# Kernel optimization log

Hardware: AMD Instinct MI355X
Metric: run time of the kernel (lower is better)

## Reference

```python
import jax, jax.numpy as jnp
import numpy as np

Z_DIM = 32
POLY_ORDER = 3
INCLUDE_BIAS = True

# Static index arrays replicating the nested-loop term ordering of the torch code.
_I2, _J2 = np.triu_indices(Z_DIM)  # pairs (i, j) with i <= j, row-major in i -> matches loop order
_TRIPLES = np.array([(i, j, k) for i in range(Z_DIM) for j in range(i, Z_DIM) for k in range(j, Z_DIM)], dtype=np.int32)
_TI, _TJ, _TK = _TRIPLES[:, 0], _TRIPLES[:, 1], _TRIPLES[:, 2]


def build_library(z):
    # z: [B, d] -> Theta: [B, n_terms], same column order as build_library_torch
    B = z.shape[0]
    terms = []
    if INCLUDE_BIAS:
        terms.append(jnp.ones((B, 1), dtype=z.dtype))
    terms.append(z)
    if POLY_ORDER >= 2:
        terms.append(z[:, _I2] * z[:, _J2])  # [B, C(d+1,2)] quadratic terms
    if POLY_ORDER >= 3:
        terms.append(z[:, _TI] * z[:, _TJ] * z[:, _TK])  # [B, C(d+2,3)] cubic terms
    return jnp.concatenate(terms, axis=1)


def setup_inputs() -> dict:
    key = jax.random.key(0)
    k1, k2 = jax.random.split(key)
    B = 65536
    n_terms = 6545  # 1 + 32 + 528 + 5984 for d=32, order=3, bias
    z = jax.random.normal(k1, (B, Z_DIM), dtype=jnp.float32)
    Xi = jax.random.normal(k2, (n_terms, Z_DIM), dtype=jnp.float32)
    Xi_mask = jnp.ones((n_terms, Z_DIM), dtype=jnp.float32)
    z_mean = jnp.zeros((1, Z_DIM), dtype=jnp.float32)
    z_std = jnp.ones((1, Z_DIM), dtype=jnp.float32)
    return {"z": z, "Xi": Xi, "Xi_mask": Xi_mask, "z_mean": z_mean, "z_std": z_std}


def reference(z, Xi, Xi_mask, z_mean, z_std):
    # NOTE: the original module computes z_norm = (z - z_mean) / z_std but
    # never uses it; Theta is built from the raw z. Reproduce exactly.
    Theta = build_library(z)            # [B, n_terms]
    Xi_eff = Xi * Xi_mask               # [n_terms, z_dim]
    dz_dt = Theta @ Xi_eff              # [B, z_dim]
    return dz_dt
```

## Files before the change

### kernel.cpp

```cpp
#include <hip/hip_runtime.h>


#define Z 32
#define ROWS 65536
#define NBLK (ROWS / 64)

#define NCHUNK 552
#define NGRAN (NCHUNK * 2)
#define NGP 1120
#define KSPAN 138

typedef short short8 __attribute__((ext_vector_type(8)));
typedef float f32x16 __attribute__((ext_vector_type(16)));
typedef float float2v __attribute__((ext_vector_type(2)));

struct Sched {
    unsigned mg[NGP];
    short rt[NGRAN * 8];
    int nq[4];
};

constexpr Sched make_sched() {
    Sched s{};
    short gi[NGP] = {}, gj[NGP] = {};
    char gt[NGP] = {}, gq[NGP] = {};
    int tidx[32][32] = {}, pidx[32] = {};
    {
        int n = 0;
        for (int a = 0; a < 32; ++a)
            for (int b = a; b < 32; ++b) { tidx[a][b] = n; n += 32 - b; }
        for (int i = 0; i < 32; ++i) pidx[i] = i * 32 - i * (i - 1) / 2;
    }
    int g = 0;
    for (int q = 0; q < 4; ++q) {
        int g0 = g;
        for (int b = 0; b < 32; ++b)
            if ((b >> 3) <= q)
                for (int a = 0; a <= b; ++a) { gi[g]=(short)a; gj[g]=(short)b; gt[g]=0; gq[g]=(char)q; ++g; }
        for (int b = 0; b < 32; ++b)
            if ((b >> 3) >= q) { gi[g]=(short)b; gj[g]=32; gt[g]=1; gq[g]=(char)q; ++g; }
        gi[g]=32; gj[g]=32; gt[g]=2; gq[g]=(char)q; ++g;
        while ((g - g0) & 7) { gi[g]=32; gj[g]=32; gt[g]=3; gq[g]=(char)q; ++g; }
        s.nq[q] = (g - g0) / 2;
    }
    for (int gg = 0; gg < NGRAN; ++gg) {
        s.mg[gg] = ((unsigned)gi[gg] * 256u) | (((unsigned)gj[gg] * 256u) << 16);
        int i = gi[gg], j = gj[gg], ty = gt[gg], q = gq[gg];
        for (int jj = 0; jj < 8; ++jj) {
            int k = 8 * q + jj, row = -1;
            if (ty == 0)      { if (k >= j) row = 561 + tidx[i][j] + (k - j); }
            else if (ty == 1) { if (k <= i) row = 33 + pidx[k] + (i - k); }
            else if (ty == 2) { row = 1 + k; }
            s.rt[gg * 8 + jj] = (short)row;
        }
    }
    return s;
}
constexpr Sched S = make_sched();
static_assert(S.nq[0] == 36 && S.nq[1] == 84 && S.nq[2] == 160 && S.nq[3] == 272, "chunk counts");

__device__ __forceinline__ unsigned pack_bf16(float s0, float s1) {
    return __builtin_amdgcn_perm(__builtin_bit_cast(unsigned, s1),
                                 __builtin_bit_cast(unsigned, s0), 0x07060302u);
}

__global__ void sindy_prep(const float* __restrict__ Xi,
                           const float* __restrict__ Xi_mask,
                           uint2* __restrict__ Bp2, size_t ws_size) {
    __shared__ unsigned short sh[8][32];
    const int tid = threadIdx.x;
    const int jj = tid >> 5, n = tid & 31;
#pragma unroll
    for (int pass = 0; pass < 4; ++pass) {
        int g = blockIdx.x * 4 + pass;
        int row = S.rt[g * 8 + jj];
        float f = 0.0f;
        if (row >= 0) f = Xi[row * Z + n] * Xi_mask[row * Z + n];
        unsigned u = __builtin_bit_cast(unsigned, f);
        sh[jj][n] = (unsigned short)((u + 0x7FFFu + ((u >> 16) & 1u)) >> 16);
        __syncthreads();
        if (tid < 64) {
            int n2 = tid & 31, rep = tid >> 5;
            unsigned v0 = sh[4*rep+0][n2], v1 = sh[4*rep+1][n2];
            unsigned v2 = sh[4*rep+2][n2], v3 = sh[4*rep+3][n2];
            int c = g >> 1, h = g & 1;
            size_t idx = ((size_t)c * 64 + h * 32 + n2) * 2 + rep;
            if ((idx + 1) * 8 <= ws_size)
                Bp2[idx] = uint2{v0 | (v1 << 16), v2 | (v3 << 16)};
        }
        __syncthreads();
    }
}

__global__ __launch_bounds__(256, 4) void sindy_mfma(const float* __restrict__ z,
                                                     const float* __restrict__ Xi,
                                                     const float* __restrict__ Xi_mask,
                                                     const uint4* __restrict__ Bp,
                                                     float* __restrict__ out) {
    const int lane = threadIdx.x & 63;
    const int kh = threadIdx.x >> 6;
    const int m = lane & 31;
    const int half = lane >> 5;
    const long R = (long)blockIdx.x * 64;

    __shared__ float zs[33][2][32];
    __shared__ float cs[3][2][32][32];
    __shared__ unsigned mg_sh[NGP];

    for (int t = threadIdx.x; t < NGP; t += 256) mg_sh[t] = S.mg[t];
    for (int idx = threadIdx.x; idx < 512; idx += 256) {
        int row = idx >> 3, q4 = idx & 7;
        float4 v = ((const float4*)(z + (R + row) * Z))[q4];
        int t = row >> 5, mm = row & 31;
        zs[4*q4+0][t][mm] = v.x; zs[4*q4+1][t][mm] = v.y;
        zs[4*q4+2][t][mm] = v.z; zs[4*q4+3][t][mm] = v.w;
    }
    if (threadIdx.x < 64) zs[32][threadIdx.x >> 5][threadIdx.x & 31] = 1.0f;
    __syncthreads();

    const int c0 = kh * KSPAN;
    const char* zmb = (const char*)&zs[0][0][0] + 4 * m;
    const unsigned* mgh = mg_sh + half;

    const uint4* p = Bp + lane + (size_t)c0 * 64;
    uint4 curA = p[0], curB = p[64];
    uint4 shA  = p[128], shB = p[192];

    unsigned u0 = mgh[2*c0], u1 = mgh[2*c0+2];
    float pA0, pA1, pB0, pB1;
    {
        float i0 = *(const float*)(zmb + (u0 & 0xFFFFu)), i1 = *(const float*)(zmb + (u0 & 0xFFFFu) + 128);
        float j0 = *(const float*)(zmb + (u0 >> 16)),     j1 = *(const float*)(zmb + (u0 >> 16) + 128);
        pA0 = i0 * j0; pA1 = i1 * j1;
        float e0 = *(const float*)(zmb + (u1 & 0xFFFFu)), e1 = *(const float*)(zmb + (u1 & 0xFFFFu) + 128);
        float f0 = *(const float*)(zmb + (u1 >> 16)),     f1 = *(const float*)(zmb + (u1 >> 16) + 128);
        pB0 = e0 * f0; pB1 = e1 * f1;
    }
    unsigned w0s = mgh[2*c0+4], w1s = mgh[2*c0+6];

    f32x16 acc0 = {}, acc1 = {};

    auto seg = [&](int Q, int cbeg, int cfin, bool lastp) {
        const char* zq = zmb + Q * 2048;
        float2v zA0, zA1, zA2, zA3, zB0, zB1, zB2, zB3;
        zA0.x = *(const float*)(zq +    0); zB0.x = *(const float*)(zq +  128);
        zA0.y = *(const float*)(zq +  256); zB0.y = *(const float*)(zq +  384);
        zA1.x = *(const float*)(zq +  512); zB1.x = *(const float*)(zq +  640);
        zA1.y = *(const float*)(zq +  768); zB1.y = *(const float*)(zq +  896);
        zA2.x = *(const float*)(zq + 1024); zB2.x = *(const float*)(zq + 1152);
        zA2.y = *(const float*)(zq + 1280); zB2.y = *(const float*)(zq + 1408);
        zA3.x = *(const float*)(zq + 1536); zB3.x = *(const float*)(zq + 1664);
        zA3.y = *(const float*)(zq + 1792); zB3.y = *(const float*)(zq + 1920);

        auto mfma0 = [&](float pp, const uint4& bv) {
            float2v p2; p2.x = pp; p2.y = pp;
            union { unsigned u[4]; short8 sv; } a;
            float2v t0 = p2 * zA0; a.u[0] = pack_bf16(t0.x, t0.y);
            float2v t1 = p2 * zA1; a.u[1] = pack_bf16(t1.x, t1.y);
            float2v t2 = p2 * zA2; a.u[2] = pack_bf16(t2.x, t2.y);
            float2v t3 = p2 * zA3; a.u[3] = pack_bf16(t3.x, t3.y);
            union { uint4 v; short8 sv; } b; b.v = bv;
            acc0 = __builtin_amdgcn_mfma_f32_32x32x16_bf16(a.sv, b.sv, acc0, 0, 0, 0);
        };
        auto mfma1 = [&](float pp, const uint4& bv) {
            float2v p2; p2.x = pp; p2.y = pp;
            union { unsigned u[4]; short8 sv; } a;
            float2v t0 = p2 * zB0; a.u[0] = pack_bf16(t0.x, t0.y);
            float2v t1 = p2 * zB1; a.u[1] = pack_bf16(t1.x, t1.y);
            float2v t2 = p2 * zB2; a.u[2] = pack_bf16(t2.x, t2.y);
            float2v t3 = p2 * zB3; a.u[3] = pack_bf16(t3.x, t3.y);
            union { uint4 v; short8 sv; } b; b.v = bv;
            acc1 = __builtin_amdgcn_mfma_f32_32x32x16_bf16(a.sv, b.sv, acc1, 0, 0, 0);
        };

        for (int c = cbeg; c < cfin; c += 2) {
            unsigned nw0 = mgh[2*c+8], nw1 = mgh[2*c+10];
            float a0i = *(const float*)(zmb + (w0s & 0xFFFFu));
            float a1i = *(const float*)(zmb + (w0s & 0xFFFFu) + 128);
            float a0j = *(const float*)(zmb + (w0s >> 16));
            float a1j = *(const float*)(zmb + (w0s >> 16) + 128);
            float b0i = *(const float*)(zmb + (w1s & 0xFFFFu));
            float b1i = *(const float*)(zmb + (w1s & 0xFFFFu) + 128);
            float b0j = *(const float*)(zmb + (w1s >> 16));
            float b1j = *(const float*)(zmb + (w1s >> 16) + 128);
            mfma0(pA0, curA); mfma1(pA1, curA);
            mfma0(pB0, curB); mfma1(pB1, curB);
            pA0 = a0i * a0j; pA1 = a1i * a1j; pB0 = b0i * b0j; pB1 = b1i * b1j;
            w0s = nw0; w1s = nw1;
            curA = shA; curB = shB;
            int off = (lastp && c + 4 >= cfin) ? 0 : 256;
            shA = p[off]; shB = p[off + 64];
            p += 128;
        }
    };

    if (kh == 0)      { seg(0,   0,  36, false); seg(1,  36, 120, false); seg(2, 120, 138, true); }
    else if (kh == 1) { seg(2, 138, 276, true); }
    else if (kh == 2) { seg(2, 276, 280, false); seg(3, 280, 414, true); }
    else              { seg(3, 414, 552, true); }

    if (kh != 0) {
#pragma unroll
        for (int r = 0; r < 16; ++r) {
            int row = (r & 3) + 8 * (r >> 2) + 4 * half;
            cs[kh - 1][0][row][m] = acc0[r];
            cs[kh - 1][1][row][m] = acc1[r];
        }
    }
    __syncthreads();
    if (kh == 0) {
        const float bias = Xi[m] * Xi_mask[m];
        float* o0 = out + R * Z;
        float* o1 = out + (R + 32) * Z;
#pragma unroll
        for (int r = 0; r < 16; ++r) {
            int row = (r & 3) + 8 * (r >> 2) + 4 * half;
            o0[row * Z + m] = acc0[r] + cs[0][0][row][m] + cs[1][0][row][m] + cs[2][0][row][m] + bias;
            o1[row * Z + m] = acc1[r] + cs[0][1][row][m] + cs[1][1][row][m] + cs[2][1][row][m] + bias;
        }
    }
}

extern "C" void kernel_launch(void* const* d_in, const int* in_sizes, int n_in,
                              void* d_out, int out_size, void* d_ws, size_t ws_size,
                              hipStream_t stream) {
    const float* z       = (const float*)d_in[0];
    const float* Xi      = (const float*)d_in[1];
    const float* Xi_mask = (const float*)d_in[2];
    float* out = (float*)d_out;
    uint4* Bp  = (uint4*)d_ws;

    sindy_prep<<<NGRAN / 4, 256, 0, stream>>>(Xi, Xi_mask, (uint2*)d_ws, ws_size);
    sindy_mfma<<<NBLK, 256, 0, stream>>>(z, Xi, Xi_mask, Bp, out);
}
```

Before: 122.3 us.

## Stream Xi operand through LDS ring via global_load_lds and serialize reduction

Replaces the register double-buffered prefetch of the packed Xi tiles with direct global-to-LDS DMA into a per-wave 4-slot ring, reading operands back from LDS each iteration. It also shrinks the cross-wave reduction buffer to one slice accumulated sequentially by waves 3,2,1. The aim is to cut register pressure and LDS footprint. In exchange it adds extra LDS reads, two barriers, and a full vmcnt wait each iteration that may expose global latency.

```diff
diff --git a/kernel.cpp b/kernel.cpp
--- a/kernel.cpp
+++ b/kernel.cpp
@@ -62,6 +62,16 @@
 __device__ __forceinline__ unsigned pack_bf16(float s0, float s1) {
     return __builtin_amdgcn_perm(__builtin_bit_cast(unsigned, s1),
                                  __builtin_bit_cast(unsigned, s0), 0x07060302u);
+}
+
+__device__ __forceinline__ void dma16(const uint4* g, uint4* lds_lane) {
+    __builtin_amdgcn_global_load_lds(
+        (const __attribute__((address_space(1))) unsigned*)g,
+        (__attribute__((address_space(3))) unsigned*)lds_lane, 16, 0, 0);
+}
+
+__device__ __forceinline__ void wait_vm0() {
+    asm volatile("s_waitcnt vmcnt(0)" ::: "memory");
 }
 
 __global__ void sindy_prep(const float* __restrict__ Xi,
@@ -104,8 +114,9 @@
     const long R = (long)blockIdx.x * 64;
 
     __shared__ float zs[33][2][32];
-    __shared__ float cs[3][2][32][32];
+    __shared__ float cs[2][32][32];
     __shared__ unsigned mg_sh[NGP];
+    __shared__ uint4 bring[4][4][64];
 
     for (int t = threadIdx.x; t < NGP; t += 256) mg_sh[t] = S.mg[t];
     for (int idx = threadIdx.x; idx < 512; idx += 256) {
@@ -121,10 +132,11 @@
     const int c0 = kh * KSPAN;
     const char* zmb = (const char*)&zs[0][0][0] + 4 * m;
     const unsigned* mgh = mg_sh + half;
-
-    const uint4* p = Bp + lane + (size_t)c0 * 64;
-    uint4 curA = p[0], curB = p[64];
-    uint4 shA  = p[128], shB = p[192];
+    const uint4* bpl = Bp + lane;
+
+    dma16(bpl + (size_t)(c0+0) * 64, &bring[kh][(c0+0) & 3][lane]);
+    dma16(bpl + (size_t)(c0+1) * 64, &bring[kh][(c0+1) & 3][lane]);
+    wait_vm0();
 
     unsigned u0 = mgh[2*c0], u1 = mgh[2*c0+2];
     float pA0, pA1, pB0, pB1;
@@ -140,7 +152,7 @@
 
     f32x16 acc0 = {}, acc1 = {};
 
-    auto seg = [&](int Q, int cbeg, int cfin, bool lastp) {
+    auto seg = [&](int Q, int cbeg, int cfin) {
         const char* zq = zmb + Q * 2048;
         float2v zA0, zA1, zA2, zA3, zB0, zB1, zB2, zB3;
         zA0.x = *(const float*)(zq +    0); zB0.x = *(const float*)(zq +  128);
@@ -174,6 +186,13 @@
         };
 
         for (int c = cbeg; c < cfin; c += 2) {
+            int l2 = c + 2, l3 = c + 3;
+            int s2 = l2 < NCHUNK ? l2 : NCHUNK - 1;
+            int s3 = l3 < NCHUNK ? l3 : NCHUNK - 1;
+            dma16(bpl + (size_t)s2 * 64, &bring[kh][l2 & 3][lane]);
+            dma16(bpl + (size_t)s3 * 64, &bring[kh][l3 & 3][lane]);
+            uint4 bA = bring[kh][c & 3][lane];
+            uint4 bB = bring[kh][(c + 1) & 3][lane];
             unsigned nw0 = mgh[2*c+8], nw1 = mgh[2*c+10];
             float a0i = *(const float*)(zmb + (w0s & 0xFFFFu));
             float a1i = *(const float*)(zmb + (w0s & 0xFFFFu) + 128);
@@ -183,28 +202,40 @@
             float b1i = *(const float*)(zmb + (w1s & 0xFFFFu) + 128);
             float b0j = *(const float*)(zmb + (w1s >> 16));
             float b1j = *(const float*)(zmb + (w1s >> 16) + 128);
-            mfma0(pA0, curA); mfma1(pA1, curA);
-            mfma0(pB0, curB); mfma1(pB1, curB);
+            mfma0(pA0, bA); mfma1(pA1, bA);
+            mfma0(pB0, bB); mfma1(pB1, bB);
             pA0 = a0i * a0j; pA1 = a1i * a1j; pB0 = b0i * b0j; pB1 = b1i * b1j;
             w0s = nw0; w1s = nw1;
-            curA = shA; curB = shB;
-            int off = (lastp && c + 4 >= cfin) ? 0 : 256;
-            shA = p[off]; shB = p[off + 64];
-            p += 128;
+            wait_vm0();
         }
     };
 
-    if (kh == 0)      { seg(0,   0,  36, false); seg(1,  36, 120, false); seg(2, 120, 138, true); }
-    else if (kh == 1) { seg(2, 138, 276, true); }
-    else if (kh == 2) { seg(2, 276, 280, false); seg(3, 280, 414, true); }
-    else              { seg(3, 414, 552, true); }
-
-    if (kh != 0) {
-#pragma unroll
-        for (int r = 0; r < 16; ++r) {
-            int row = (r & 3) + 8 * (r >> 2) + 4 * half;
-            cs[kh - 1][0][row][m] = acc0[r];
-            cs[kh - 1][1][row][m] = acc1[r];
+    if (kh == 0)      { seg(0,   0,  36); seg(1,  36, 120); seg(2, 120, 138); }
+    else if (kh == 1) { seg(2, 138, 276); }
+    else if (kh == 2) { seg(2, 276, 280); seg(3, 280, 414); }
+    else              { seg(3, 414, 552); }
+
+    if (kh == 3) {
+#pragma unroll
+        for (int r = 0; r < 16; ++r) {
+            int row = (r & 3) + 8 * (r >> 2) + 4 * half;
+            cs[0][row][m] = acc0[r]; cs[1][row][m] = acc1[r];
+        }
+    }
+    __syncthreads();
+    if (kh == 2) {
+#pragma unroll
+        for (int r = 0; r < 16; ++r) {
+            int row = (r & 3) + 8 * (r >> 2) + 4 * half;
+            cs[0][row][m] += acc0[r]; cs[1][row][m] += acc1[r];
+        }
+    }
+    __syncthreads();
+    if (kh == 1) {
+#pragma unroll
+        for (int r = 0; r < 16; ++r) {
+            int row = (r & 3) + 8 * (r >> 2) + 4 * half;
+            cs[0][row][m] += acc0[r]; cs[1][row][m] += acc1[r];
         }
     }
     __syncthreads();
@@ -215,8 +246,8 @@
 #pragma unroll
         for (int r = 0; r < 16; ++r) {
             int row = (r & 3) + 8 * (r >> 2) + 4 * half;
-            o0[row * Z + m] = acc0[r] + cs[0][0][row][m] + cs[1][0][row][m] + cs[2][0][row][m] + bias;
-            o1[row * Z + m] = acc1[r] + cs[0][1][row][m] + cs[1][1][row][m] + cs[2][1][row][m] + bias;
+            o0[row * Z + m] = acc0[r] + cs[0][row][m] + bias;
+            o1[row * Z + m] = acc1[r] + cs[1][row][m] + bias;
         }
     }
 }
```

Result: no change. 121.6 us (-0.6%).
